# Optimization experiments

Hardware: AMD Instinct MI355X
Metric: run time of the kernel (lower is better)

Reference implementation:

```python
import jax, jax.numpy as jnp
import numpy as np

NB_CLASSES = 10  # matches init_kwargs nb_classes


def setup_inputs() -> dict:
    key = jax.random.key(0)
    k1, k2 = jax.random.split(key)
    N, D = 500_000, 64
    h = jax.random.normal(k1, (N, D), dtype=jnp.float32)
    yhat = jax.random.randint(k2, (N,), 0, NB_CLASSES, dtype=jnp.int32)
    return {"h": h, "yhat": yhat}


def reference(h, yhat):
    # Original torch loop: for each class k, gather h_k = h[yhat==k],
    # M_k = mean_i(h_i h_i^T) * 0.5 + I, loss += 0.5 * logdet(M_k).
    # mean of outer products == (masked h)^T @ h / count_k, so we avoid
    # the ragged gather and any [N, D, D] intermediate entirely.
    N, D = h.shape
    eye = jnp.eye(D, dtype=h.dtype)

    def class_term(k):
        mask = (yhat == k).astype(h.dtype)            # [N]
        count = jnp.sum(mask)                         # B_k
        gram = jnp.einsum('nd,ne->de', mask[:, None] * h, h)  # sum_i h_i h_i^T
        M = gram * (0.5 / count) + eye                # [D, D], SPD
        _, logabsdet = jnp.linalg.slogdet(M)
        return 0.5 * logabsdet

    # NB_CLASSES is a small fixed constant -> Python loop is fine & keeps
    # peak memory at one extra [N, D] buffer.
    return jnp.sum(jnp.stack([class_term(k) for k in range(NB_CLASSES)]))
```

## Files before the change

kernel.cpp:

```cpp
#include <hip/hip_runtime.h>
#include <hip/hip_bf16.h>

typedef __attribute__((ext_vector_type(8))) short  short8;
typedef __attribute__((ext_vector_type(4))) float  f32x4;

#define NCLS 10
#define TILE 128
#define TPB  1024
#define NQ   10
#define PPB  (NCLS * NQ * 256)
#define CH   16

#define AS1 __attribute__((address_space(1)))
#define AS3 __attribute__((address_space(3)))

static __device__ inline unsigned short f2bf(float x) {
    unsigned u = __builtin_bit_cast(unsigned, x);
    return (unsigned short)((u + 0x7FFFu + ((u >> 16) & 1u)) >> 16);
}

static __device__ __forceinline__ void issue_tile(
        const float* __restrict__ h, const int* __restrict__ yhat,
        float* fsb, int* yb, long t, long N, int wid, int lane) {
#pragma unroll
    for (int i = 0; i < 2; ++i) {
        const int C  = wid * 128 + i * 64 + lane;
        const int n  = C >> 4;
        const int cc = C & 15;
        long row = t * TILE + n;
        if (row > N - 1) row = N - 1;
        const float* gp = h + row * 64 + ((cc << 2) ^ ((n & 7) << 3));
        __builtin_amdgcn_global_load_lds((const AS1 float*)gp,
                                         (AS3 float*)(fsb + (wid * 2 + i) * 256),
                                         16, 0, 0);
    }
    if (wid == 0 && lane < 32) {
        long y0 = t * TILE + lane * 4;
        if (y0 > N - 4) y0 = N - 4;
        __builtin_amdgcn_global_load_lds((const AS1 int*)(yhat + y0),
                                         (AS3 int*)yb, 16, 0, 0);
    }
}

template<int NS>
static __device__ __forceinline__ void compute_range(
        const char* hsb, const char* mkb,
        int cls, int ks0, int hi, int col, f32x4 (&acc)[NQ]) {
    const int cb = col << 8;
    const int c7 = col & 7;
#pragma unroll
    for (int s = 0; s < NS; ++s) {
        const int ks = ks0 + s;
        const short8 m = *reinterpret_cast<const short8*>(mkb + cls * 256 + ks * 64 + hi * 16);
        const int x = ((ks * 4 + hi) ^ c7) << 4;
        short8 am[4];
#pragma unroll
        for (int nb = 0; nb < 4; ++nb) {
            short8 r = *reinterpret_cast<const short8*>(hsb + nb * 4096 + cb + x);
            am[nb] = r & m;
        }
        acc[0] = __builtin_amdgcn_mfma_f32_16x16x32_bf16(am[0], am[0], acc[0], 0, 0, 0);
        acc[1] = __builtin_amdgcn_mfma_f32_16x16x32_bf16(am[0], am[1], acc[1], 0, 0, 0);
        acc[2] = __builtin_amdgcn_mfma_f32_16x16x32_bf16(am[0], am[2], acc[2], 0, 0, 0);
        acc[3] = __builtin_amdgcn_mfma_f32_16x16x32_bf16(am[0], am[3], acc[3], 0, 0, 0);
        acc[4] = __builtin_amdgcn_mfma_f32_16x16x32_bf16(am[1], am[1], acc[4], 0, 0, 0);
        acc[5] = __builtin_amdgcn_mfma_f32_16x16x32_bf16(am[1], am[2], acc[5], 0, 0, 0);
        acc[6] = __builtin_amdgcn_mfma_f32_16x16x32_bf16(am[1], am[3], acc[6], 0, 0, 0);
        acc[7] = __builtin_amdgcn_mfma_f32_16x16x32_bf16(am[2], am[2], acc[7], 0, 0, 0);
        acc[8] = __builtin_amdgcn_mfma_f32_16x16x32_bf16(am[2], am[3], acc[8], 0, 0, 0);
        acc[9] = __builtin_amdgcn_mfma_f32_16x16x32_bf16(am[3], am[3], acc[9], 0, 0, 0);
    }
}

__global__ __launch_bounds__(TPB, 4) void HL_gram(
        const float* __restrict__ h, const int* __restrict__ yhat,
        float* __restrict__ partials, int* __restrict__ cntp,
        long N, int ntiles, int G) {
    __shared__ __align__(16) float          fs[3][TILE * 64];
    __shared__ __align__(16) unsigned short hs[2][64 * TILE];
    __shared__ __align__(16) unsigned short mk[2][NCLS * TILE];
    __shared__ __align__(16) int            ylds[3][TILE];
    __shared__ int cntlds[16];

    const int tid  = threadIdx.x;
    const int wid  = tid >> 6;
    const int lane = tid & 63;
    const int hi   = lane >> 4;
    const int col  = lane & 15;

    if (tid < 16) cntlds[tid] = 0;
    asm volatile("s_waitcnt lgkmcnt(0)" ::: "memory");

    int cls, ks0, ns;
    if      (wid < 6)  { cls = wid;      ks0 = 0; ns = 2; }
    else if (wid < 10) { cls = wid;      ks0 = 0; ns = 4; }
    else               { cls = wid - 10; ks0 = 2; ns = 2; }

    f32x4 acc[NQ];
#pragma unroll
    for (int q = 0; q < NQ; ++q) acc[q] = (f32x4){0.f, 0.f, 0.f, 0.f};

    const int bid = blockIdx.x;
    const int K   = (ntiles - bid + G - 1) / G;

#pragma unroll
    for (int kk = 0; kk < 3; ++kk)
        if (kk < K)
            issue_tile(h, yhat, &fs[kk][0], &ylds[kk][0], bid + (long)kk * G, N, wid, lane);

    for (int k = 0; k < K; ++k) {
        const long t  = bid + (long)k * G;
        const int  bk = k % 3;
        const int  hk = k & 1;
        const int  r  = (K - 1 - k) > 2 ? 2 : (K - 1 - k);

        if (wid == 0) {
            if (r == 2)      asm volatile("s_waitcnt vmcnt(6)" ::: "memory");
            else if (r == 1) asm volatile("s_waitcnt vmcnt(3)" ::: "memory");
            else             asm volatile("s_waitcnt vmcnt(0)" ::: "memory");
        } else {
            if (r == 2)      asm volatile("s_waitcnt vmcnt(4)" ::: "memory");
            else if (r == 1) asm volatile("s_waitcnt vmcnt(2)" ::: "memory");
            else             asm volatile("s_waitcnt vmcnt(0)" ::: "memory");
        }
        __builtin_amdgcn_s_barrier();

        {
            const float* fsb = &fs[bk][0];
            short8 w;
#pragma unroll
            for (int j = 0; j < 8; ++j) {
                const float x = fsb[(wid * 8 + j) * 64 + (lane ^ (j << 3))];
                w[j] = (short)f2bf(x);
            }
            *reinterpret_cast<short8*>(
                (char*)&hs[hk][0] + lane * 256 + ((wid ^ (lane & 7)) << 4)) = w;
        }
        if (tid < TILE) {
            int y = ylds[bk][tid];
            if (t * TILE + tid >= N) y = -1;
#pragma unroll
            for (int c = 0; c < NCLS; ++c) {
                mk[hk][c * TILE + tid] = (y == c) ? (unsigned short)0xFFFFu : (unsigned short)0u;
                unsigned long long b = __ballot(y == c);
                if (lane == 0) atomicAdd(&cntlds[c], __popcll(b));
            }
        }

        asm volatile("s_waitcnt lgkmcnt(0)" ::: "memory");
        __builtin_amdgcn_s_barrier();

        if (k + 3 < K)
            issue_tile(h, yhat, &fs[bk][0], &ylds[bk][0], bid + (long)(k + 3) * G, N, wid, lane);

        if (ns == 4) compute_range<4>((const char*)&hs[hk][0], (const char*)&mk[hk][0],
                                      cls, 0,   hi, col, acc);
        else         compute_range<2>((const char*)&hs[hk][0], (const char*)&mk[hk][0],
                                      cls, ks0, hi, col, acc);
    }

    float* xch = (float*)&fs[0][0];
#pragma unroll
    for (int qq = 0; qq < NQ; qq += 2) {
        __syncthreads();
        if (wid >= 10) {
            float* dst = xch + (wid - 10) * 512;
            *reinterpret_cast<f32x4*>(dst + (lane << 2))       = acc[qq];
            *reinterpret_cast<f32x4*>(dst + 256 + (lane << 2)) = acc[qq + 1];
        }
        __syncthreads();
        if (wid < 6) {
            const float* src = xch + wid * 512;
            acc[qq]     += *reinterpret_cast<const f32x4*>(src + (lane << 2));
            acc[qq + 1] += *reinterpret_cast<const f32x4*>(src + 256 + (lane << 2));
        }
    }

    if (wid < NCLS) {
        float* pb = partials + (size_t)bid * PPB + (size_t)wid * (NQ * 256);
#pragma unroll
        for (int q = 0; q < NQ; ++q)
            *reinterpret_cast<f32x4*>(pb + q * 256 + (lane << 2)) = acc[q];
    }
    if (tid < NCLS) cntp[bid * 16 + tid] = cntlds[tid];
}

__global__ void HL_reduce(const float* __restrict__ partials, float* __restrict__ rpart,
                          float* __restrict__ out, int G, int CS) {
    const int idx = blockIdx.x * blockDim.x + threadIdx.x;
    if (blockIdx.x == 0 && threadIdx.x == 0) out[0] = 0.f;
    if (idx >= CH * NCLS * NQ * 64) return;
    const int ch = idx / (NCLS * NQ * 64);
    const int r  = idx % (NCLS * NQ * 64);
    const int cq = r >> 6;
    const int l  = r & 63;

    int b0 = ch * CS;
    int b1 = b0 + CS; if (b1 > G) b1 = G;

    f32x4 s = (f32x4){0.f, 0.f, 0.f, 0.f};
    const float* p = partials + (size_t)cq * 256 + (l << 2);
    for (int b = b0; b < b1; ++b)
        s += *reinterpret_cast<const f32x4*>(p + (size_t)b * PPB);

    *reinterpret_cast<f32x4*>(rpart + ((size_t)ch * (NCLS * NQ) + cq) * 256 + (l << 2)) = s;
}

__global__ __launch_bounds__(64, 1) void HL_chol(
        const float* __restrict__ rpart, const int* __restrict__ cntp,
        float* __restrict__ out, int G) {
    __shared__ float M[64][68];
    __shared__ float lcol[64];
    const int cls = blockIdx.x;
    const int i   = threadIdx.x;

    int c = 0;
    for (int b = i; b < G; b += 64) c += cntp[b * 16 + cls];
#pragma unroll
    for (int off = 32; off > 0; off >>= 1) c += __shfl_xor(c, off);
    const float inv = 0.5f / (float)c;

    const int QMB[NQ] = {0,0,0,0,1,1,1,2,2,3};
    const int QNB[NQ] = {0,1,2,3,1,2,3,2,3,3};
    const float* rp = rpart + (size_t)cls * (NQ * 256);
#pragma unroll
    for (int q = 0; q < NQ; ++q) {
        f32x4 s = (f32x4){0.f, 0.f, 0.f, 0.f};
#pragma unroll
        for (int ch = 0; ch < CH; ++ch)
            s += *reinterpret_cast<const f32x4*>(rp + (size_t)ch * (NCLS * NQ * 256) + q * 256 + (i << 2));
        const int row0 = QMB[q] * 16 + ((i >> 4) << 2);
        const int colo = QNB[q] * 16 + (i & 15);
#pragma unroll
        for (int rr = 0; rr < 4; ++rr) {
            M[row0 + rr][colo] = s[rr];
            M[colo][row0 + rr] = s[rr];
        }
    }
    __syncthreads();

    float row[64];
#pragma unroll
    for (int c2 = 0; c2 < 64; ++c2)
        row[c2] = M[i][c2] * inv + (c2 == i ? 1.0f : 0.0f);

#pragma unroll
    for (int j = 0; j < 64; ++j) {
        const float piv = __shfl(row[j], j);
        const float li  = row[j] * rsqrtf(piv);
        lcol[i] = li;
        __syncthreads();
#pragma unroll
        for (int c2 = j + 1; c2 < 64; ++c2)
            row[c2] -= li * lcol[c2];
        __syncthreads();
    }

    float slog = 0.f;
#pragma unroll
    for (int j = 0; j < 64; ++j)
        if (i == j) slog = __logf(row[j]);
    slog += __shfl_down(slog, 32); slog += __shfl_down(slog, 16);
    slog += __shfl_down(slog, 8);  slog += __shfl_down(slog, 4);
    slog += __shfl_down(slog, 2);  slog += __shfl_down(slog, 1);
    if (i == 0) atomicAdd(out, 0.5f * slog);
}

extern "C" void kernel_launch(void* const* d_in, const int* in_sizes, int n_in,
                              void* d_out, int out_size, void* d_ws, size_t ws_size,
                              hipStream_t stream) {
    const float* h    = (const float*)d_in[0];
    const int*   yhat = (const int*)d_in[1];
    const long   N    = in_sizes[1];
    float* out = (float*)d_out;

    const size_t rpart_sz = (size_t)CH * NCLS * NQ * 256 * sizeof(float);
    const size_t cntp_off = rpart_sz;

    const int ntiles = (int)((N + TILE - 1) / TILE);
    int G = 256;
    {
        const size_t perG = 64 + (size_t)PPB * sizeof(float);
        if (ws_size > rpart_sz) {
            size_t maxG = (ws_size - rpart_sz) / perG;
            if ((size_t)G > maxG) G = (int)maxG;
        } else G = 1;
        if (G < 1) G = 1;
    }
    if (G > ntiles) G = ntiles;

    const size_t partials_off = cntp_off + (size_t)G * 16 * sizeof(int);
    float* rpart    = (float*)d_ws;
    int*   cntp     = (int*)((char*)d_ws + cntp_off);
    float* partials = (float*)((char*)d_ws + partials_off);

    HL_gram<<<G, TPB, 0, stream>>>(h, yhat, partials, cntp, N, ntiles, G);

    int CS = (G + CH - 1) / CH;
    const int rthreads = CH * NCLS * NQ * 64;
    HL_reduce<<<(rthreads + 255) / 256, 256, 0, stream>>>(partials, rpart, out, G, CS);

    HL_chol<<<NCLS, 64, 0, stream>>>(rpart, cntp, out, G);
}
```

Baseline: 83.79 us.

## Rework gram kernel to 8-wave blocks with 96-row tiles and split class work

After: 91.83 us. 1.1x slower.

```diff
diff --git a/kernel.cpp b/kernel.cpp
--- a/kernel.cpp
+++ b/kernel.cpp
@@ -5,8 +5,8 @@
 typedef __attribute__((ext_vector_type(4))) float  f32x4;
 
 #define NCLS 10
-#define TILE 128
-#define TPB  1024
+#define TILE 96
+#define TPB  512
 #define NQ   10
 #define PPB  (NCLS * NQ * 256)
 #define CH   16
@@ -14,6 +14,8 @@
 #define AS1 __attribute__((address_space(1)))
 #define AS3 __attribute__((address_space(3)))
 
+#define MF(a, b, c) __builtin_amdgcn_mfma_f32_16x16x32_bf16((a), (b), (c), 0, 0, 0)
+
 static __device__ inline unsigned short f2bf(float x) {
     unsigned u = __builtin_bit_cast(unsigned, x);
     return (unsigned short)((u + 0x7FFFu + ((u >> 16) & 1u)) >> 16);
@@ -23,18 +25,16 @@
         const float* __restrict__ h, const int* __restrict__ yhat,
         float* fsb, int* yb, long t, long N, int wid, int lane) {
 #pragma unroll
-    for (int i = 0; i < 2; ++i) {
-        const int C  = wid * 128 + i * 64 + lane;
-        const int n  = C >> 4;
-        const int cc = C & 15;
-        long row = t * TILE + n;
+    for (int i = 0; i < 3; ++i) {
+        const int C = wid * 64 + i * 512 + lane;
+        long row = t * TILE + (C >> 4);
         if (row > N - 1) row = N - 1;
-        const float* gp = h + row * 64 + ((cc << 2) ^ ((n & 7) << 3));
+        const float* gp = h + row * 64 + ((C & 15) << 2);
         __builtin_amdgcn_global_load_lds((const AS1 float*)gp,
-                                         (AS3 float*)(fsb + (wid * 2 + i) * 256),
+                                         (AS3 float*)(fsb + (wid * 64 + i * 512) * 4),
                                          16, 0, 0);
     }
-    if (wid == 0 && lane < 32) {
+    if (wid == 0 && lane < 24) {
         long y0 = t * TILE + lane * 4;
         if (y0 > N - 4) y0 = N - 4;
         __builtin_amdgcn_global_load_lds((const AS1 int*)(yhat + y0),
@@ -42,33 +42,48 @@
     }
 }
 
-template<int NS>
-static __device__ __forceinline__ void compute_range(
-        const char* hsb, const char* mkb,
-        int cls, int ks0, int hi, int col, f32x4 (&acc)[NQ]) {
-    const int cb = col << 8;
-    const int c7 = col & 7;
-#pragma unroll
-    for (int s = 0; s < NS; ++s) {
-        const int ks = ks0 + s;
-        const short8 m = *reinterpret_cast<const short8*>(mkb + cls * 256 + ks * 64 + hi * 16);
-        const int x = ((ks * 4 + hi) ^ c7) << 4;
-        short8 am[4];
+static __device__ __forceinline__ void compute_tile(
+        const char* hsb, const unsigned short* mkb, int cls, int xcls, int wq,
+        int hi, int col, f32x4 (&acc)[NQ], f32x4 (&accx)[3]) {
+    const int sw = (col & 3) << 4;
+#pragma unroll
+    for (int ks = 0; ks < 3; ++ks) {
+        const int b2 = ks * 64 + hi * 16;
+        const short8 m = *(const short8*)((const char*)mkb + cls * 192 + b2);
+        short8 raw[4], am[4];
 #pragma unroll
         for (int nb = 0; nb < 4; ++nb) {
-            short8 r = *reinterpret_cast<const short8*>(hsb + nb * 4096 + cb + x);
-            am[nb] = r & m;
-        }
-        acc[0] = __builtin_amdgcn_mfma_f32_16x16x32_bf16(am[0], am[0], acc[0], 0, 0, 0);
-        acc[1] = __builtin_amdgcn_mfma_f32_16x16x32_bf16(am[0], am[1], acc[1], 0, 0, 0);
-        acc[2] = __builtin_amdgcn_mfma_f32_16x16x32_bf16(am[0], am[2], acc[2], 0, 0, 0);
-        acc[3] = __builtin_amdgcn_mfma_f32_16x16x32_bf16(am[0], am[3], acc[3], 0, 0, 0);
-        acc[4] = __builtin_amdgcn_mfma_f32_16x16x32_bf16(am[1], am[1], acc[4], 0, 0, 0);
-        acc[5] = __builtin_amdgcn_mfma_f32_16x16x32_bf16(am[1], am[2], acc[5], 0, 0, 0);
-        acc[6] = __builtin_amdgcn_mfma_f32_16x16x32_bf16(am[1], am[3], acc[6], 0, 0, 0);
-        acc[7] = __builtin_amdgcn_mfma_f32_16x16x32_bf16(am[2], am[2], acc[7], 0, 0, 0);
-        acc[8] = __builtin_amdgcn_mfma_f32_16x16x32_bf16(am[2], am[3], acc[8], 0, 0, 0);
-        acc[9] = __builtin_amdgcn_mfma_f32_16x16x32_bf16(am[3], am[3], acc[9], 0, 0, 0);
+            raw[nb] = *(const short8*)(hsb + (nb * 16 + col) * 192 + (b2 ^ sw));
+            am[nb]  = raw[nb] & m;
+        }
+        acc[0] = MF(am[0], am[0], acc[0]);
+        acc[1] = MF(am[0], am[1], acc[1]);
+        acc[2] = MF(am[0], am[2], acc[2]);
+        acc[3] = MF(am[0], am[3], acc[3]);
+        acc[4] = MF(am[1], am[1], acc[4]);
+        acc[5] = MF(am[1], am[2], acc[5]);
+        acc[6] = MF(am[1], am[3], acc[6]);
+        acc[7] = MF(am[2], am[2], acc[7]);
+        acc[8] = MF(am[2], am[3], acc[8]);
+        acc[9] = MF(am[3], am[3], acc[9]);
+
+        const short8 mx = *(const short8*)((const char*)mkb + xcls * 192 + b2);
+        switch (wq) {
+        case 0: { short8 x0 = raw[0] & mx, x1 = raw[1] & mx;
+                  accx[0] = MF(x0, x0, accx[0]);
+                  accx[1] = MF(x0, x1, accx[1]);
+                  accx[2] = MF(x1, x1, accx[2]); } break;
+        case 1: { short8 x0 = raw[0] & mx, x2 = raw[2] & mx, x3 = raw[3] & mx;
+                  accx[0] = MF(x0, x2, accx[0]);
+                  accx[1] = MF(x0, x3, accx[1]); } break;
+        case 2: { short8 x1 = raw[1] & mx, x2 = raw[2] & mx, x3 = raw[3] & mx;
+                  accx[0] = MF(x1, x2, accx[0]);
+                  accx[1] = MF(x1, x3, accx[1]);
+                  accx[2] = MF(x2, x2, accx[2]); } break;
+        default:{ short8 x2 = raw[2] & mx, x3 = raw[3] & mx;
+                  accx[0] = MF(x2, x3, accx[0]);
+                  accx[1] = MF(x3, x3, accx[1]); } break;
+        }
     }
 }
 
@@ -76,10 +91,10 @@
         const float* __restrict__ h, const int* __restrict__ yhat,
         float* __restrict__ partials, int* __restrict__ cntp,
         long N, int ntiles, int G) {
-    __shared__ __align__(16) float          fs[3][TILE * 64];
-    __shared__ __align__(16) unsigned short hs[2][64 * TILE];
-    __shared__ __align__(16) unsigned short mk[2][NCLS * TILE];
-    __shared__ __align__(16) int            ylds[3][TILE];
+    __shared__ __align__(16) float          fs[2][TILE * 64];
+    __shared__ __align__(16) unsigned short hs[64 * TILE];
+    __shared__ __align__(16) unsigned short mk[NCLS * TILE];
+    __shared__ __align__(16) int            ylds[2][TILE];
     __shared__ int cntlds[16];
 
     const int tid  = threadIdx.x;
@@ -88,101 +103,101 @@
     const int hi   = lane >> 4;
     const int col  = lane & 15;
 
+    const int cls  = wid;
+    const int xcls = 8 + (wid >> 2);
+    const int wq   = wid & 3;
+
     if (tid < 16) cntlds[tid] = 0;
-    asm volatile("s_waitcnt lgkmcnt(0)" ::: "memory");
-
-    int cls, ks0, ns;
-    if      (wid < 6)  { cls = wid;      ks0 = 0; ns = 2; }
-    else if (wid < 10) { cls = wid;      ks0 = 0; ns = 4; }
-    else               { cls = wid - 10; ks0 = 2; ns = 2; }
-
-    f32x4 acc[NQ];
+    __syncthreads();
+
+    f32x4 acc[NQ], accx[3];
 #pragma unroll
     for (int q = 0; q < NQ; ++q) acc[q] = (f32x4){0.f, 0.f, 0.f, 0.f};
+#pragma unroll
+    for (int q = 0; q < 3; ++q)  accx[q] = (f32x4){0.f, 0.f, 0.f, 0.f};
 
     const int bid = blockIdx.x;
     const int K   = (ntiles - bid + G - 1) / G;
 
-#pragma unroll
-    for (int kk = 0; kk < 3; ++kk)
-        if (kk < K)
-            issue_tile(h, yhat, &fs[kk][0], &ylds[kk][0], bid + (long)kk * G, N, wid, lane);
+    issue_tile(h, yhat, &fs[0][0], &ylds[0][0], bid, N, wid, lane);
+    if (K > 1)
+        issue_tile(h, yhat, &fs[1][0], &ylds[1][0], bid + (long)G, N, wid, lane);
 
     for (int k = 0; k < K; ++k) {
         const long t  = bid + (long)k * G;
-        const int  bk = k % 3;
-        const int  hk = k & 1;
-        const int  r  = (K - 1 - k) > 2 ? 2 : (K - 1 - k);
-
-        if (wid == 0) {
-            if (r == 2)      asm volatile("s_waitcnt vmcnt(6)" ::: "memory");
-            else if (r == 1) asm volatile("s_waitcnt vmcnt(3)" ::: "memory");
-            else             asm volatile("s_waitcnt vmcnt(0)" ::: "memory");
+        const int  bk = k & 1;
+
+        if (k + 1 < K) {
+            if (wid == 0) asm volatile("s_waitcnt vmcnt(4)" ::: "memory");
+            else          asm volatile("s_waitcnt vmcnt(3)" ::: "memory");
         } else {
-            if (r == 2)      asm volatile("s_waitcnt vmcnt(4)" ::: "memory");
-            else if (r == 1) asm volatile("s_waitcnt vmcnt(2)" ::: "memory");
-            else             asm volatile("s_waitcnt vmcnt(0)" ::: "memory");
+            asm volatile("s_waitcnt vmcnt(0)" ::: "memory");
         }
         __builtin_amdgcn_s_barrier();
 
-        {
-            const float* fsb = &fs[bk][0];
-            short8 w;
-#pragma unroll
-            for (int j = 0; j < 8; ++j) {
-                const float x = fsb[(wid * 8 + j) * 64 + (lane ^ (j << 3))];
-                w[j] = (short)f2bf(x);
-            }
-            *reinterpret_cast<short8*>(
-                (char*)&hs[hk][0] + lane * 256 + ((wid ^ (lane & 7)) << 4)) = w;
-        }
-        if (tid < TILE) {
-            int y = ylds[bk][tid];
-            if (t * TILE + tid >= N) y = -1;
-#pragma unroll
-            for (int c = 0; c < NCLS; ++c) {
-                mk[hk][c * TILE + tid] = (y == c) ? (unsigned short)0xFFFFu : (unsigned short)0u;
-                unsigned long long b = __ballot(y == c);
-                if (lane == 0) atomicAdd(&cntlds[c], __popcll(b));
+        if (tid < 384) {
+            const int d  = lane;
+            const int r0 = wid * 16;
+            const float* fp = &fs[bk][0] + r0 * 64 + d;
+            short8 w0, w1;
+#pragma unroll
+            for (int j = 0; j < 8; ++j) w0[j] = (short)f2bf(fp[j * 64]);
+#pragma unroll
+            for (int j = 0; j < 8; ++j) w1[j] = (short)f2bf(fp[(j + 8) * 64]);
+            const int sw = (d & 3) << 4;
+            char* hb = (char*)hs + d * 192;
+            *(short8*)(hb + ((r0 * 2)      ^ sw)) = w0;
+            *(short8*)(hb + ((r0 * 2 + 16) ^ sw)) = w1;
+        } else {
+            const int r = (wid - 6) * 64 + lane;
+            if (r < TILE) {
+                const long grow = t * TILE + r;
+                const int y = (grow < N) ? ylds[bk][r] : -1;
+#pragma unroll
+                for (int c = 0; c < NCLS; ++c) {
+                    mk[c * TILE + r] = (y == c) ? (unsigned short)0xFFFFu
+                                                : (unsigned short)0u;
+                    unsigned long long b = __ballot(y == c);
+                    if (lane == 0) atomicAdd(&cntlds[c], __popcll(b));
+                }
             }
         }
 
         asm volatile("s_waitcnt lgkmcnt(0)" ::: "memory");
         __builtin_amdgcn_s_barrier();
 
-        if (k + 3 < K)
-            issue_tile(h, yhat, &fs[bk][0], &ylds[bk][0], bid + (long)(k + 3) * G, N, wid, lane);
-
-        if (ns == 4) compute_range<4>((const char*)&hs[hk][0], (const char*)&mk[hk][0],
-                                      cls, 0,   hi, col, acc);
-        else         compute_range<2>((const char*)&hs[hk][0], (const char*)&mk[hk][0],
-                                      cls, ks0, hi, col, acc);
-    }
-
-    float* xch = (float*)&fs[0][0];
-#pragma unroll
-    for (int qq = 0; qq < NQ; qq += 2) {
-        __syncthreads();
-        if (wid >= 10) {
-            float* dst = xch + (wid - 10) * 512;
-            *reinterpret_cast<f32x4*>(dst + (lane << 2))       = acc[qq];
-            *reinterpret_cast<f32x4*>(dst + 256 + (lane << 2)) = acc[qq + 1];
-        }
-        __syncthreads();
-        if (wid < 6) {
-            const float* src = xch + wid * 512;
-            acc[qq]     += *reinterpret_cast<const f32x4*>(src + (lane << 2));
-            acc[qq + 1] += *reinterpret_cast<const f32x4*>(src + 256 + (lane << 2));
-        }
-    }
-
-    if (wid < NCLS) {
-        float* pb = partials + (size_t)bid * PPB + (size_t)wid * (NQ * 256);
+        if (k + 2 < K)
+            issue_tile(h, yhat, &fs[bk][0], &ylds[bk][0],
+                       bid + (long)(k + 2) * G, N, wid, lane);
+
+        compute_tile((const char*)hs, mk, cls, xcls, wq, hi, col, acc, accx);
+    }
+
+    __syncthreads();
+
+    float* pb = partials + (size_t)bid * PPB;
+    {
+        float* po = pb + (size_t)cls * (NQ * 256);
 #pragma unroll
         for (int q = 0; q < NQ; ++q)
-            *reinterpret_cast<f32x4*>(pb + q * 256 + (lane << 2)) = acc[q];
-    }
-    if (tid < NCLS) cntp[bid * 16 + tid] = cntlds[tid];
+            *(f32x4*)(po + q * 256 + (lane << 2)) = acc[q];
+    }
+    {
+        float* px = pb + (size_t)xcls * (NQ * 256) + (lane << 2);
+        switch (wq) {
+        case 0: *(f32x4*)(px + 0 * 256) = accx[0];
+                *(f32x4*)(px + 1 * 256) = accx[1];
+                *(f32x4*)(px + 4 * 256) = accx[2]; break;
+        case 1: *(f32x4*)(px + 2 * 256) = accx[0];
+                *(f32x4*)(px + 3 * 256) = accx[1]; break;
+        case 2: *(f32x4*)(px + 5 * 256) = accx[0];
+                *(f32x4*)(px + 6 * 256) = accx[1];
+                *(f32x4*)(px + 7 * 256) = accx[2]; break;
+        default:*(f32x4*)(px + 8 * 256) = accx[0];
+                *(f32x4*)(px + 9 * 256) = accx[1]; break;
+        }
+    }
+    if (tid < 16) cntp[bid * 16 + tid] = cntlds[tid];
 }
 
 __global__ void HL_reduce(const float* __restrict__ partials, float* __restrict__ rpart,
@@ -278,7 +293,7 @@
     const size_t cntp_off = rpart_sz;
 
     const int ntiles = (int)((N + TILE - 1) / TILE);
-    int G = 256;
+    int G = 512;
     {
         const size_t perG = 64 + (size_t)PPB * sizeof(float);
         if (ws_size > rpart_sz) {
```
